# Kernel optimization log

Hardware: AMD Instinct MI355X
Metric: run time of the kernel (lower is better)

Reference implementation:

```python
import jax, jax.numpy as jnp
import numpy as np

B, T, U = 32, 512, 64
V, H, E = 32000, 512, 512


def setup_inputs() -> dict:
    key = jax.random.key(0)
    ks = jax.random.split(key, 12)
    s = 0.02
    return {
        "encoder_out": jax.random.normal(ks[0], (B, T, E), jnp.float32),
        "encoder_lens": jax.random.randint(ks[1], (B,), 1, T + 1),
        "decoder_in": jax.random.randint(ks[2], (B, U), 0, V),
        "emb_table": jax.random.normal(ks[3], (V, H), jnp.float32) * s,
        "W_attn": jax.random.normal(ks[4], (H, E), jnp.float32) * s,
        "W_ih0": jax.random.normal(ks[5], (3 * H, H + E), jnp.float32) * s,
        "W_hh0": jax.random.normal(ks[6], (3 * H, H), jnp.float32) * s,
        "b_ih0": jnp.zeros((3 * H,), jnp.float32),
        "b_hh0": jnp.zeros((3 * H,), jnp.float32),
        "W_ih1": jax.random.normal(ks[7], (3 * H, H), jnp.float32) * s,
        "W_hh1": jax.random.normal(ks[8], (3 * H, H), jnp.float32) * s,
        "b_ih1": jnp.zeros((3 * H,), jnp.float32),
        "b_hh1": jnp.zeros((3 * H,), jnp.float32),
        "W_out": jax.random.normal(ks[9], (V, H + E), jnp.float32) * s,
        "b_out": jnp.zeros((V,), jnp.float32),
    }


def gru_cell(x, h, W_ih, W_hh, b_ih, b_hh):
    # PyTorch GRUCell gate math
    gi = x @ W_ih.T + b_ih          # [B, 3H]
    gh = h @ W_hh.T + b_hh          # [B, 3H]
    i_r, i_z, i_n = jnp.split(gi, 3, axis=-1)
    h_r, h_z, h_n = jnp.split(gh, 3, axis=-1)
    r = jax.nn.sigmoid(i_r + h_r)
    z = jax.nn.sigmoid(i_z + h_z)
    n = jnp.tanh(i_n + r * h_n)
    return (1.0 - z) * n + z * h


def reference(encoder_out, encoder_lens, decoder_in, emb_table, W_attn,
              W_ih0, W_hh0, b_ih0, b_hh0, W_ih1, W_hh1, b_ih1, b_hh1,
              W_out, b_out):
    b, t_max, e = encoder_out.shape
    u_max = decoder_in.shape[1]
    enc_proj = jnp.einsum('bte,he->bth', encoder_out, W_attn)   # [B,T,H]
    embedded = emb_table[decoder_in]                            # [B,U,H]
    pad_mask = jnp.arange(t_max)[None, :] >= encoder_lens[:, None]  # [B,T]
    h_dim = emb_table.shape[1]

    def step(carry, xs):
        h0, h1 = carry
        emb_t, t = xs                                           # emb_t: [B,H]
        # first step: query is the embedding; afterwards: top-layer hidden
        query = jnp.where(t == 0, emb_t, h1)
        scores = jnp.einsum('bth,bh->bt', enc_proj, query)      # [B,T]
        scores = jnp.where(pad_mask, -jnp.inf, scores)
        attn = jax.nn.softmax(scores, axis=1)
        context = jnp.einsum('bt,bte->be', attn, encoder_out)   # [B,E]
        x = jnp.concatenate([emb_t, context], axis=-1)          # [B,H+E]
        h0n = gru_cell(x, h0, W_ih0, W_hh0, b_ih0, b_hh0)
        h1n = gru_cell(h0n, h1, W_ih1, W_hh1, b_ih1, b_hh1)     # dropout=eval mode (no-op)
        logits = jnp.concatenate([h1n, context], axis=-1) @ W_out.T + b_out  # [B,V]
        return (h0n, h1n), logits

    init = (jnp.zeros((b, h_dim), encoder_out.dtype),
            jnp.zeros((b, h_dim), encoder_out.dtype))
    xs = (jnp.swapaxes(embedded, 0, 1), jnp.arange(u_max))
    _, logits = jax.lax.scan(step, init, xs)                    # [U,B,V]
    return jnp.swapaxes(logits, 0, 1)                           # [B,U,V]
```

## Files before the change

### kernel.cpp

```cpp
#include <hip/hip_runtime.h>
#include <math.h>

#define B_ 32
#define T_ 512
#define U_ 64
#define V_ 32000
#define H_ 512
#define E_ 512

__global__ void embed_kernel(const int* __restrict__ tok, const float* __restrict__ table,
                             float* __restrict__ out) {
  int row = blockIdx.x;
  int t = tok[row];
  const float4* src = (const float4*)(table + (size_t)t * H_);
  float4* dst = (float4*)(out + (size_t)row * H_);
  dst[threadIdx.x] = src[threadIdx.x];
}

__global__ void zero_kernel(float* p, int n) {
  int i = blockIdx.x * blockDim.x + threadIdx.x;
  if (i < n) p[i] = 0.f;
}

__global__ __launch_bounds__(256) void gemm_abt(
    const float* __restrict__ A, const float* __restrict__ Bm,
    const float* __restrict__ bias, float* __restrict__ C,
    int N, int K, int lda, int ldb) {
  __shared__ float As[8][128];
  __shared__ float Bs[8][128];
  int tid = threadIdx.x;
  int n0 = blockIdx.x * 128, m0 = blockIdx.y * 128;
  int lr = tid >> 1;
  int lk = (tid & 1) * 4;
  const float* Ap = A + (size_t)(m0 + lr) * lda + lk;
  const float* Bp = Bm + (size_t)(n0 + lr) * ldb + lk;
  int tx = tid & 15, ty = tid >> 4;
  float acc[8][8];
#pragma unroll
  for (int i = 0; i < 8; i++)
#pragma unroll
    for (int j = 0; j < 8; j++) acc[i][j] = 0.f;

  for (int k0 = 0; k0 < K; k0 += 8) {
    float4 av = *(const float4*)(Ap + k0);
    float4 bv = *(const float4*)(Bp + k0);
    __syncthreads();
    As[lk + 0][lr] = av.x; As[lk + 1][lr] = av.y; As[lk + 2][lr] = av.z; As[lk + 3][lr] = av.w;
    Bs[lk + 0][lr] = bv.x; Bs[lk + 1][lr] = bv.y; Bs[lk + 2][lr] = bv.z; Bs[lk + 3][lr] = bv.w;
    __syncthreads();
#pragma unroll
    for (int kk = 0; kk < 8; kk++) {
      float a[8], b[8];
      *(float4*)&a[0] = *(const float4*)&As[kk][ty * 4];
      *(float4*)&a[4] = *(const float4*)&As[kk][ty * 4 + 64];
      *(float4*)&b[0] = *(const float4*)&Bs[kk][tx * 4];
      *(float4*)&b[4] = *(const float4*)&Bs[kk][tx * 4 + 64];
#pragma unroll
      for (int i = 0; i < 8; i++)
#pragma unroll
        for (int j = 0; j < 8; j++) acc[i][j] = fmaf(a[i], b[j], acc[i][j]);
    }
  }
  float bb[8] = {0, 0, 0, 0, 0, 0, 0, 0};
  if (bias) {
    *(float4*)&bb[0] = *(const float4*)&bias[n0 + tx * 4];
    *(float4*)&bb[4] = *(const float4*)&bias[n0 + tx * 4 + 64];
  }
#pragma unroll
  for (int i = 0; i < 8; i++) {
    int m = m0 + ty * 4 + (i & 3) + (i >> 2) * 64;
    float* Crow = C + (size_t)m * N + n0;
    float4 o0 = make_float4(acc[i][0] + bb[0], acc[i][1] + bb[1], acc[i][2] + bb[2], acc[i][3] + bb[3]);
    float4 o1 = make_float4(acc[i][4] + bb[4], acc[i][5] + bb[5], acc[i][6] + bb[6], acc[i][7] + bb[7]);
    *(float4*)(Crow + tx * 4) = o0;
    *(float4*)(Crow + tx * 4 + 64) = o1;
  }
}

__global__ __launch_bounds__(512) void attn_scores(
    const float* __restrict__ enc_proj, const int* __restrict__ lens,
    const float* __restrict__ embedded, const float* __restrict__ h1_prev,
    float* __restrict__ sc_raw, int u) {
  int s = blockIdx.x, b = blockIdx.y;
  int tid = threadIdx.x;
  __shared__ __align__(16) float q[H_];
  q[tid] = (u == 0) ? embedded[((size_t)b * U_ + u) * H_ + tid] : h1_prev[b * H_ + tid];
  __syncthreads();
  int len = lens[b];
  int w = tid >> 6, l = tid & 63;
  int t0 = s * 64 + w * 8;
  const float4* q4 = (const float4*)q;
  float4 b0 = q4[l], b1 = q4[l + 64];
#pragma unroll
  for (int i = 0; i < 8; i++) {
    int t = t0 + i;
    if (t < len) {
      const float4* r4 = (const float4*)(enc_proj + ((size_t)b * T_ + t) * H_);
      float4 a0 = r4[l], a1 = r4[l + 64];
      float acc = a0.x * b0.x + a0.y * b0.y + a0.z * b0.z + a0.w * b0.w
                + a1.x * b1.x + a1.y * b1.y + a1.z * b1.z + a1.w * b1.w;
#pragma unroll
      for (int off = 32; off > 0; off >>= 1) acc += __shfl_xor(acc, off, 64);
      if (l == 0) sc_raw[b * T_ + t] = acc;
    } else {
      if (l == 0) sc_raw[b * T_ + t] = -INFINITY;
    }
  }
}

__global__ __launch_bounds__(512) void attn_ctx(
    const float* __restrict__ enc_out, const float* __restrict__ sc_raw,
    float* __restrict__ X, int u) {
  int s = blockIdx.x, b = blockIdx.y;
  int tid = threadIdx.x;
  __shared__ float p[T_];
  __shared__ float red[512];
  float v = sc_raw[b * T_ + tid];
  red[tid] = v;
  __syncthreads();
  for (int st = 256; st > 0; st >>= 1) { if (tid < st) red[tid] = fmaxf(red[tid], red[tid + st]); __syncthreads(); }
  float mx = red[0];
  __syncthreads();
  float e = expf(v - mx);
  red[tid] = e;
  __syncthreads();
  for (int st = 256; st > 0; st >>= 1) { if (tid < st) red[tid] += red[tid + st]; __syncthreads(); }
  float inv = 1.f / red[0];
  __syncthreads();
  p[tid] = e * inv;
  __syncthreads();
  int l = tid & 63, stripe = tid >> 6;
  const float* eo = enc_out + (size_t)b * T_ * E_ + s * 64 + l;
  float a0 = 0, a1 = 0, a2 = 0, a3 = 0, a4 = 0, a5 = 0, a6 = 0, a7 = 0;
  for (int t = stripe; t < T_; t += 64) {
    a0 += p[t]      * eo[(size_t)(t)      * E_];
    a1 += p[t +  8] * eo[(size_t)(t +  8) * E_];
    a2 += p[t + 16] * eo[(size_t)(t + 16) * E_];
    a3 += p[t + 24] * eo[(size_t)(t + 24) * E_];
    a4 += p[t + 32] * eo[(size_t)(t + 32) * E_];
    a5 += p[t + 40] * eo[(size_t)(t + 40) * E_];
    a6 += p[t + 48] * eo[(size_t)(t + 48) * E_];
    a7 += p[t + 56] * eo[(size_t)(t + 56) * E_];
  }
  red[tid] = a0 + a1 + a2 + a3 + a4 + a5 + a6 + a7;
  __syncthreads();
  if (tid < 64) {
    float r = red[tid];
#pragma unroll
    for (int i = 1; i < 8; i++) r += red[tid + 64 * i];
    X[((size_t)b * U_ + u) * (H_ + E_) + H_ + s * 64 + tid] = r;
  }
}

__global__ __launch_bounds__(256) void gru0_step(
    const float* __restrict__ X, const float* __restrict__ GI0,
    const float* __restrict__ h_prev, const float* __restrict__ W_ih,
    const float* __restrict__ W_hh, const float* __restrict__ b_ih,
    const float* __restrict__ b_hh, float* __restrict__ h_next, int u) {
  int j = blockIdx.x;
  int tid = threadIdx.x;
  __shared__ __align__(16) float Wr[512], Wz[512], Wn[512], Vr[512], Vz[512], Vn[512];
  __shared__ float red[4][256];
  {
    int h2 = tid & 127;
    const float4* wr4 = (const float4*)(W_ih + (size_t)j * 1024 + 512);
    const float4* wz4 = (const float4*)(W_ih + ((size_t)j + 512) * 1024 + 512);
    const float4* wn4 = (const float4*)(W_ih + ((size_t)j + 1024) * 1024 + 512);
    const float4* vr4 = (const float4*)(W_hh + (size_t)j * 512);
    const float4* vz4 = (const float4*)(W_hh + ((size_t)j + 512) * 512);
    const float4* vn4 = (const float4*)(W_hh + ((size_t)j + 1024) * 512);
    if (tid < 128) {
      ((float4*)Wr)[h2] = wr4[h2];
      ((float4*)Wn)[h2] = wn4[h2];
      ((float4*)Vz)[h2] = vz4[h2];
    } else {
      ((float4*)Wz)[h2] = wz4[h2];
      ((float4*)Vr)[h2] = vr4[h2];
      ((float4*)Vn)[h2] = vn4[h2];
    }
  }
  __syncthreads();
  int b = tid >> 3, s = tid & 7;
  const float4* xc = (const float4*)(X + ((size_t)b * U_ + u) * (H_ + E_) + H_);
  const float4* hp = (const float4*)(h_prev + (size_t)b * H_);
  float ar = 0, az = 0, ain = 0, ahn = 0;
#pragma unroll 4
  for (int i = 0; i < 16; i++) {
    int k4 = s + i * 8;
    float4 xv = xc[k4];
    float4 hv = hp[k4];
    float4 wr = ((const float4*)Wr)[k4];
    float4 wz = ((const float4*)Wz)[k4];
    float4 wn = ((const float4*)Wn)[k4];
    float4 vr = ((const float4*)Vr)[k4];
    float4 vz = ((const float4*)Vz)[k4];
    float4 vn = ((const float4*)Vn)[k4];
    ar += wr.x * xv.x + wr.y * xv.y + wr.z * xv.z + wr.w * xv.w
        + vr.x * hv.x + vr.y * hv.y + vr.z * hv.z + vr.w * hv.w;
    az += wz.x * xv.x + wz.y * xv.y + wz.z * xv.z + wz.w * xv.w
        + vz.x * hv.x + vz.y * hv.y + vz.z * hv.z + vz.w * hv.w;
    ain += wn.x * xv.x + wn.y * xv.y + wn.z * xv.z + wn.w * xv.w;
    ahn += vn.x * hv.x + vn.y * hv.y + vn.z * hv.z + vn.w * hv.w;
  }
  red[0][tid] = ar; red[1][tid] = az; red[2][tid] = ain; red[3][tid] = ahn;
  __syncthreads();
  if (tid < 32) {
    int bb = tid;
    float r = 0, z = 0, in_ = 0, hn = 0;
#pragma unroll
    for (int q2 = 0; q2 < 8; q2++) {
      r += red[0][bb * 8 + q2]; z += red[1][bb * 8 + q2];
      in_ += red[2][bb * 8 + q2]; hn += red[3][bb * 8 + q2];
    }
    size_t grow = ((size_t)bb * U_ + u) * 1536;
    r += GI0[grow + j] + b_ih[j] + b_hh[j];
    z += GI0[grow + 512 + j] + b_ih[512 + j] + b_hh[512 + j];
    in_ += GI0[grow + 1024 + j];
    float rg = 1.f / (1.f + expf(-r));
    float zg = 1.f / (1.f + expf(-z));
    float n = tanhf(in_ + b_ih[1024 + j] + rg * (hn + b_hh[1024 + j]));
    h_next[bb * H_ + j] = (1.f - zg) * n + zg * h_prev[bb * H_ + j];
  }
}

__global__ __launch_bounds__(256) void gru1_step(
    const float* __restrict__ xin, const float* __restrict__ h_prev,
    const float* __restrict__ W_ih, const float* __restrict__ W_hh,
    const float* __restrict__ b_ih, const float* __restrict__ b_hh,
    float* __restrict__ h_next, float* __restrict__ X, int u) {
  int j = blockIdx.x;
  int tid = threadIdx.x;
  __shared__ __align__(16) float Wr[512], Wz[512], Wn[512], Vr[512], Vz[512], Vn[512];
  __shared__ float red[4][256];
  {
    int h2 = tid & 127;
    const float4* wr4 = (const float4*)(W_ih + (size_t)j * 512);
    const float4* wz4 = (const float4*)(W_ih + ((size_t)j + 512) * 512);
    const float4* wn4 = (const float4*)(W_ih + ((size_t)j + 1024) * 512);
    const float4* vr4 = (const float4*)(W_hh + (size_t)j * 512);
    const float4* vz4 = (const float4*)(W_hh + ((size_t)j + 512) * 512);
    const float4* vn4 = (const float4*)(W_hh + ((size_t)j + 1024) * 512);
    if (tid < 128) {
      ((float4*)Wr)[h2] = wr4[h2];
      ((float4*)Wn)[h2] = wn4[h2];
      ((float4*)Vz)[h2] = vz4[h2];
    } else {
      ((float4*)Wz)[h2] = wz4[h2];
      ((float4*)Vr)[h2] = vr4[h2];
      ((float4*)Vn)[h2] = vn4[h2];
    }
  }
  __syncthreads();
  int b = tid >> 3, s = tid & 7;
  const float4* xp = (const float4*)(xin + (size_t)b * H_);
  const float4* hp = (const float4*)(h_prev + (size_t)b * H_);
  float ar = 0, az = 0, ain = 0, ahn = 0;
#pragma unroll 4
  for (int i = 0; i < 16; i++) {
    int k4 = s + i * 8;
    float4 xv = xp[k4];
    float4 hv = hp[k4];
    float4 wr = ((const float4*)Wr)[k4];
    float4 wz = ((const float4*)Wz)[k4];
    float4 wn = ((const float4*)Wn)[k4];
    float4 vr = ((const float4*)Vr)[k4];
    float4 vz = ((const float4*)Vz)[k4];
    float4 vn = ((const float4*)Vn)[k4];
    ar += wr.x * xv.x + wr.y * xv.y + wr.z * xv.z + wr.w * xv.w
        + vr.x * hv.x + vr.y * hv.y + vr.z * hv.z + vr.w * hv.w;
    az += wz.x * xv.x + wz.y * xv.y + wz.z * xv.z + wz.w * xv.w
        + vz.x * hv.x + vz.y * hv.y + vz.z * hv.z + vz.w * hv.w;
    ain += wn.x * xv.x + wn.y * xv.y + wn.z * xv.z + wn.w * xv.w;
    ahn += vn.x * hv.x + vn.y * hv.y + vn.z * hv.z + vn.w * hv.w;
  }
  red[0][tid] = ar; red[1][tid] = az; red[2][tid] = ain; red[3][tid] = ahn;
  __syncthreads();
  if (tid < 32) {
    int bb = tid;
    float r = 0, z = 0, in_ = 0, hn = 0;
#pragma unroll
    for (int q2 = 0; q2 < 8; q2++) {
      r += red[0][bb * 8 + q2]; z += red[1][bb * 8 + q2];
      in_ += red[2][bb * 8 + q2]; hn += red[3][bb * 8 + q2];
    }
    r += b_ih[j] + b_hh[j];
    z += b_ih[512 + j] + b_hh[512 + j];
    float rg = 1.f / (1.f + expf(-r));
    float zg = 1.f / (1.f + expf(-z));
    float n = tanhf(in_ + b_ih[1024 + j] + rg * (hn + b_hh[1024 + j]));
    float ho = (1.f - zg) * n + zg * h_prev[bb * H_ + j];
    h_next[bb * H_ + j] = ho;
    X[((size_t)bb * U_ + u) * (H_ + E_) + j] = ho;
  }
}

extern "C" void kernel_launch(void* const* d_in, const int* in_sizes, int n_in,
                              void* d_out, int out_size, void* d_ws, size_t ws_size,
                              hipStream_t stream) {
  const float* encoder_out  = (const float*)d_in[0];
  const int*   encoder_lens = (const int*)d_in[1];
  const int*   decoder_in   = (const int*)d_in[2];
  const float* emb_table    = (const float*)d_in[3];
  const float* W_attn       = (const float*)d_in[4];
  const float* W_ih0        = (const float*)d_in[5];
  const float* W_hh0        = (const float*)d_in[6];
  const float* b_ih0        = (const float*)d_in[7];
  const float* b_hh0        = (const float*)d_in[8];
  const float* W_ih1        = (const float*)d_in[9];
  const float* W_hh1        = (const float*)d_in[10];
  const float* b_ih1        = (const float*)d_in[11];
  const float* b_hh1        = (const float*)d_in[12];
  const float* W_out        = (const float*)d_in[13];
  const float* b_out        = (const float*)d_in[14];
  float* out = (float*)d_out;

  float* X   = (float*)d_ws;
  float* h0b = X + 2097152;
  float* h1b = h0b + 32768;
  float* enc_proj = out;
  float* embedded = out + 8388608;
  float* GI0      = out + 9437184;
  float* sc_raw   = out + 12582912;

  zero_kernel<<<256, 256, 0, stream>>>(h0b, 65536);
  embed_kernel<<<B_ * U_, 128, 0, stream>>>(decoder_in, emb_table, embedded);
  gemm_abt<<<dim3(4, 128), 256, 0, stream>>>(encoder_out, W_attn, nullptr, enc_proj, 512, 512, 512, 512);
  gemm_abt<<<dim3(12, 16), 256, 0, stream>>>(embedded, W_ih0, nullptr, GI0, 1536, 512, 512, 1024);

  for (int u = 0; u < U_; u++) {
    int cur = u & 1, nxt = cur ^ 1;
    attn_scores<<<dim3(8, B_), 512, 0, stream>>>(enc_proj, encoder_lens, embedded,
                                                 h1b + cur * 16384, sc_raw, u);
    attn_ctx<<<dim3(8, B_), 512, 0, stream>>>(encoder_out, sc_raw, X, u);
    gru0_step<<<512, 256, 0, stream>>>(X, GI0, h0b + cur * 16384, W_ih0, W_hh0,
                                       b_ih0, b_hh0, h0b + nxt * 16384, u);
    gru1_step<<<512, 256, 0, stream>>>(h0b + nxt * 16384, h1b + cur * 16384, W_ih1, W_hh1,
                                       b_ih1, b_hh1, h1b + nxt * 16384, X, u);
  }
  gemm_abt<<<dim3(250, 16), 256, 0, stream>>>(X, W_out, b_out, out, V_, 1024, 1024, 1024);
}
```

Measured before the change: 4.705 ms.

## Run output projection on bf16x3 MFMA with split-precision packed operands

Replaces the final fp32 SIMT GEMM (X @ W_out^T) with an MFMA kernel that splits each fp32 value into bf16 high and low halves and accumulates three bf16 products to recover near-fp32 accuracy. W_out and X are first packed into hi/lo 32-bit words in workspace, and the shared-memory tiles use an XOR swizzle. This moves the dominant FLOPs onto matrix cores, at the cost of an extra pass over the 131MB W_out each call, triple the MFMA count, and a fallback that depends on workspace size.

Result: faster. 3.864 ms (-17.9%).

```diff
diff --git a/kernel.cpp b/kernel.cpp
--- a/kernel.cpp
+++ b/kernel.cpp
@@ -7,6 +7,9 @@
 #define V_ 32000
 #define H_ 512
 #define E_ 512
+
+typedef short short8 __attribute__((ext_vector_type(8)));
+typedef float f32x4 __attribute__((ext_vector_type(4)));
 
 __global__ void embed_kernel(const int* __restrict__ tok, const float* __restrict__ table,
                              float* __restrict__ out) {
@@ -22,6 +25,24 @@
   if (i < n) p[i] = 0.f;
 }
 
+__device__ __forceinline__ unsigned pack1(float f) {
+  unsigned u = __float_as_uint(f);
+  unsigned hi = u & 0xffff0000u;
+  float lo = f - __uint_as_float(hi);
+  return hi | (__float_as_uint(lo) >> 16);
+}
+
+__global__ __launch_bounds__(256) void pack_kernel(const float4* __restrict__ src,
+                                                   uint4* __restrict__ dst, int n4) {
+  int i = blockIdx.x * blockDim.x + threadIdx.x;
+  if (i < n4) {
+    float4 f = src[i];
+    uint4 o;
+    o.x = pack1(f.x); o.y = pack1(f.y); o.z = pack1(f.z); o.w = pack1(f.w);
+    dst[i] = o;
+  }
+}
+
 __global__ __launch_bounds__(256) void gemm_abt(
     const float* __restrict__ A, const float* __restrict__ Bm,
     const float* __restrict__ bias, float* __restrict__ C,
@@ -74,6 +95,84 @@
     float4 o1 = make_float4(acc[i][4] + bb[4], acc[i][5] + bb[5], acc[i][6] + bb[6], acc[i][7] + bb[7]);
     *(float4*)(Crow + tx * 4) = o0;
     *(float4*)(Crow + tx * 4 + 64) = o1;
+  }
+}
+
+__device__ __forceinline__ void unpack8(uint4 u0, uint4 u1, short8& h, short8& l) {
+  h[0] = (short)(u0.x >> 16); l[0] = (short)(u0.x & 0xffffu);
+  h[1] = (short)(u0.y >> 16); l[1] = (short)(u0.y & 0xffffu);
+  h[2] = (short)(u0.z >> 16); l[2] = (short)(u0.z & 0xffffu);
+  h[3] = (short)(u0.w >> 16); l[3] = (short)(u0.w & 0xffffu);
+  h[4] = (short)(u1.x >> 16); l[4] = (short)(u1.x & 0xffffu);
+  h[5] = (short)(u1.y >> 16); l[5] = (short)(u1.y & 0xffffu);
+  h[6] = (short)(u1.z >> 16); l[6] = (short)(u1.z & 0xffffu);
+  h[7] = (short)(u1.w >> 16); l[7] = (short)(u1.w & 0xffffu);
+}
+
+__global__ __launch_bounds__(256) void gemm_mfma(
+    const unsigned* __restrict__ Ap, const unsigned* __restrict__ Bp,
+    const float* __restrict__ bias, float* __restrict__ C, int N, int K) {
+  __shared__ __align__(16) unsigned As[128 * 64];
+  __shared__ __align__(16) unsigned Bs[128 * 64];
+  int tid = threadIdx.x;
+  int n0 = blockIdx.x * 128, m0 = blockIdx.y * 128;
+  int w = tid >> 6, l = tid & 63;
+  int wm = (w >> 1) * 64, wn = (w & 1) * 64;
+  f32x4 acc[4][4];
+#pragma unroll
+  for (int i = 0; i < 4; i++)
+#pragma unroll
+    for (int j = 0; j < 4; j++) acc[i][j] = (f32x4){0.f, 0.f, 0.f, 0.f};
+
+  for (int kt = 0; kt < K; kt += 64) {
+    __syncthreads();
+#pragma unroll
+    for (int i = 0; i < 8; i++) {
+      int off16 = tid + i * 256;
+      int row = off16 >> 4, c = off16 & 15;
+      int sc = c ^ (row & 15);
+      *(uint4*)&As[(size_t)off16 * 4] = *(const uint4*)&Ap[(size_t)(m0 + row) * K + kt + sc * 4];
+      *(uint4*)&Bs[(size_t)off16 * 4] = *(const uint4*)&Bp[(size_t)(n0 + row) * K + kt + sc * 4];
+    }
+    __syncthreads();
+#pragma unroll
+    for (int kk = 0; kk < 2; kk++) {
+      short8 ah[4], al[4], bh[4], bl[4];
+      int c0 = kk * 8 + (l >> 4) * 2;
+#pragma unroll
+      for (int fm = 0; fm < 4; fm++) {
+        int row = wm + fm * 16 + (l & 15);
+        uint4 u0 = *(const uint4*)&As[(row * 16 + (c0 ^ (row & 15))) * 4];
+        uint4 u1 = *(const uint4*)&As[(row * 16 + ((c0 + 1) ^ (row & 15))) * 4];
+        unpack8(u0, u1, ah[fm], al[fm]);
+      }
+#pragma unroll
+      for (int fn = 0; fn < 4; fn++) {
+        int row = wn + fn * 16 + (l & 15);
+        uint4 u0 = *(const uint4*)&Bs[(row * 16 + (c0 ^ (row & 15))) * 4];
+        uint4 u1 = *(const uint4*)&Bs[(row * 16 + ((c0 + 1) ^ (row & 15))) * 4];
+        unpack8(u0, u1, bh[fn], bl[fn]);
+      }
+#pragma unroll
+      for (int fm = 0; fm < 4; fm++)
+#pragma unroll
+        for (int fn = 0; fn < 4; fn++) {
+          acc[fm][fn] = __builtin_amdgcn_mfma_f32_16x16x32_bf16(ah[fm], bh[fn], acc[fm][fn], 0, 0, 0);
+          acc[fm][fn] = __builtin_amdgcn_mfma_f32_16x16x32_bf16(ah[fm], bl[fn], acc[fm][fn], 0, 0, 0);
+          acc[fm][fn] = __builtin_amdgcn_mfma_f32_16x16x32_bf16(al[fm], bh[fn], acc[fm][fn], 0, 0, 0);
+        }
+    }
+  }
+#pragma unroll
+  for (int fn = 0; fn < 4; fn++) {
+    int n = n0 + wn + fn * 16 + (l & 15);
+    float bz = bias ? bias[n] : 0.f;
+#pragma unroll
+    for (int fm = 0; fm < 4; fm++) {
+      int mbase = m0 + wm + fm * 16 + (l >> 4) * 4;
+#pragma unroll
+      for (int r = 0; r < 4; r++) C[(size_t)(mbase + r) * N + n] = acc[fm][fn][r] + bz;
+    }
   }
 }
 
@@ -317,6 +416,11 @@
   float* X   = (float*)d_ws;
   float* h0b = X + 2097152;
   float* h1b = h0b + 32768;
+  unsigned* Xpack = (unsigned*)(h1b + 32768);
+  unsigned* Wpack = Xpack + 2097152;
+  size_t ws_need = ((size_t)2097152 + 65536 + 2097152 + 32768000) * 4;
+  bool use_mfma = ws_size >= ws_need;
+
   float* enc_proj = out;
   float* embedded = out + 8388608;
   float* GI0      = out + 9437184;
@@ -326,6 +430,9 @@
   embed_kernel<<<B_ * U_, 128, 0, stream>>>(decoder_in, emb_table, embedded);
   gemm_abt<<<dim3(4, 128), 256, 0, stream>>>(encoder_out, W_attn, nullptr, enc_proj, 512, 512, 512, 512);
   gemm_abt<<<dim3(12, 16), 256, 0, stream>>>(embedded, W_ih0, nullptr, GI0, 1536, 512, 512, 1024);
+  if (use_mfma) {
+    pack_kernel<<<32000, 256, 0, stream>>>((const float4*)W_out, (uint4*)Wpack, 8192000);
+  }
 
   for (int u = 0; u < U_; u++) {
     int cur = u & 1, nxt = cur ^ 1;
@@ -337,5 +444,10 @@
     gru1_step<<<512, 256, 0, stream>>>(h0b + nxt * 16384, h1b + cur * 16384, W_ih1, W_hh1,
                                        b_ih1, b_hh1, h1b + nxt * 16384, X, u);
   }
-  gemm_abt<<<dim3(250, 16), 256, 0, stream>>>(X, W_out, b_out, out, V_, 1024, 1024, 1024);
-}
+  if (use_mfma) {
+    pack_kernel<<<2048, 256, 0, stream>>>((const float4*)X, (uint4*)Xpack, 524288);
+    gemm_mfma<<<dim3(250, 16), 256, 0, stream>>>(Xpack, Wpack, b_out, out, V_, 1024);
+  } else {
+    gemm_abt<<<dim3(250, 16), 256, 0, stream>>>(X, W_out, b_out, out, V_, 1024, 1024, 1024);
+  }
+}
```
